# Performance work log

Measured on AMD Instinct MI355X. Metric: run time of the kernel, lower is better.

## Reference

```python
import jax, jax.numpy as jnp
import numpy as np

D_MODEL = 1024
NUM_HEADS = 16
HEAD_DIM = D_MODEL // NUM_HEADS
B, L = 2, 2048


def apply_rope(x, pos_emb):
    # x: [B,H,L,Dh], pos_emb: [1,1,L,Dh]
    x_even = x[..., ::2]
    x_odd = x[..., 1::2]
    cos = pos_emb[..., ::2]
    sin = pos_emb[..., 1::2]
    return jnp.concatenate([x_even * cos - x_odd * sin,
                            x_even * sin + x_odd * cos], axis=-1)


def setup_inputs() -> dict:
    key = jax.random.key(0)
    ks = jax.random.split(key, 13)
    s = D_MODEL ** -0.5
    return {
        'query': jax.random.normal(ks[0], (B, L, D_MODEL), jnp.float32),
        'key': jax.random.normal(ks[1], (B, L, D_MODEL), jnp.float32),
        'value': jax.random.normal(ks[2], (B, L, D_MODEL), jnp.float32),
        'alibi_bias': jax.random.normal(ks[3], (NUM_HEADS, L, L), jnp.float32),
        'pos_emb': jax.random.normal(ks[4], (1, 1, L, HEAD_DIM), jnp.float32),
        'Wq': jax.random.normal(ks[5], (D_MODEL, D_MODEL), jnp.float32) * s,
        'bq': jnp.zeros((D_MODEL,), jnp.float32),
        'Wk': jax.random.normal(ks[6], (D_MODEL, D_MODEL), jnp.float32) * s,
        'bk': jnp.zeros((D_MODEL,), jnp.float32),
        'Wv': jax.random.normal(ks[7], (D_MODEL, D_MODEL), jnp.float32) * s,
        'bv': jnp.zeros((D_MODEL,), jnp.float32),
        'Wo': jax.random.normal(ks[8], (D_MODEL, D_MODEL), jnp.float32) * s,
        'bo': jnp.zeros((D_MODEL,), jnp.float32),
    }


def reference(query, key, value, alibi_bias, pos_emb,
              Wq, bq, Wk, bk, Wv, bv, Wo, bo):
    scaling = HEAD_DIM ** -0.5
    Bq, Lq, _ = query.shape

    def proj(x, W, b):
        # torch Linear: x @ W.T + b -> [B,H,L,Dh]
        y = x @ W.T + b
        return y.reshape(Bq, Lq, NUM_HEADS, HEAD_DIM).transpose(0, 2, 1, 3)

    q = proj(query, Wq, bq)
    k = proj(key, Wk, bk)
    v = proj(value, Wv, bv)

    q = apply_rope(q, pos_emb)
    k = apply_rope(k, pos_emb)

    scores = jnp.einsum('bhqd,bhkd->bhqk', q, k) * scaling
    scores = scores + alibi_bias[None]
    attn = jax.nn.softmax(scores, axis=-1)
    out = jnp.einsum('bhqk,bhkd->bhqd', attn, v)
    out = out.transpose(0, 2, 1, 3).reshape(Bq, Lq, D_MODEL)
    return out @ Wo.T + bo
```

## Files before the change

### kernel.cpp

```cpp
#include <hip/hip_runtime.h>
#include <hip/hip_bf16.h>

#define DM 1024
#define NH 16
#define HD 64
#define BB 2
#define LLEN 2048
#define MR (BB*LLEN)

typedef __attribute__((ext_vector_type(8))) short bf16x8;
typedef __attribute__((ext_vector_type(4))) float f32x4;

#define AS1(p) ((const __attribute__((address_space(1))) void*)(p))
#define AS3(p) ((__attribute__((address_space(3))) void*)(p))

__device__ __forceinline__ ushort f2bf(float x) {
    union { float f; unsigned u; } v; v.f = x;
    unsigned r = v.u + 0x7FFFu + ((v.u >> 16) & 1u);
    return (ushort)(r >> 16);
}
__device__ __forceinline__ float bf2f(ushort x) {
    union { unsigned u; float f; } v; v.u = ((unsigned)x) << 16;
    return v.f;
}

__global__ __launch_bounds__(256) void cvtX(const float* __restrict__ a,
                                            const float* __restrict__ b,
                                            const float* __restrict__ c,
                                            ushort* __restrict__ dst, int n) {
    const float* src = blockIdx.y == 0 ? a : (blockIdx.y == 1 ? b : c);
    ushort* d = dst + (size_t)blockIdx.y * n;
    int i = (blockIdx.x * 256 + threadIdx.x) * 4;
    float4 v = *(const float4*)(src + i);
    ushort4 o = make_ushort4(f2bf(v.x), f2bf(v.y), f2bf(v.z), f2bf(v.w));
    *(ushort4*)(d + i) = o;
}

__global__ __launch_bounds__(256) void cvtW(const float* __restrict__ w0,
                                            const float* __restrict__ w1,
                                            const float* __restrict__ w2,
                                            const float* __restrict__ w3,
                                            ushort* __restrict__ dst, int n) {
    const float* src = blockIdx.y == 0 ? w0 : (blockIdx.y == 1 ? w1 : (blockIdx.y == 2 ? w2 : w3));
    ushort* d = dst + (size_t)blockIdx.y * n;
    int i = (blockIdx.x * 256 + threadIdx.x) * 4;
    float4 v = *(const float4*)(src + i);
    ushort4 o = make_ushort4(f2bf(v.x), f2bf(v.y), f2bf(v.z), f2bf(v.w));
    *(ushort4*)(d + i) = o;
}

template<typename OutT>
__global__ __launch_bounds__(256) void gemm_bt(
    const ushort* __restrict__ A, const ushort* __restrict__ Bw,
    OutT* __restrict__ Cc,
    const float* __restrict__ bias0, const float* __restrict__ bias1, const float* __restrict__ bias2,
    int M, int N, int K, long sA, long sB, long sC)
{
    __shared__ __attribute__((aligned(16))) ushort As[128 * 32];
    __shared__ __attribute__((aligned(16))) ushort Bs[128 * 32];
    const int tid = threadIdx.x;
    const int lane = tid & 63;
    const int wv = tid >> 6;
    const int wm = wv >> 1, wn = wv & 1;
    const int z = blockIdx.z;
    const ushort* Ab = A + (size_t)z * sA;
    const ushort* Bb = Bw + (size_t)z * sB;
    OutT* Cb = Cc + (size_t)z * sC;
    const float* bias = z == 0 ? bias0 : (z == 1 ? bias1 : bias2);
    const int m0 = blockIdx.x * 128;
    const int n0 = blockIdx.y * 128;
    const int l15 = lane & 15, l4 = lane >> 4;

    f32x4 acc[4][4] = {};
    const int nk = K >> 5;
    const int srow = tid >> 2;
    const int sblk = tid & 3;

    auto stage = [&](int kb) {
        int k0 = kb * 32;
#pragma unroll
        for (int r = 0; r < 2; ++r) {
            int row = r * 64 + srow;
            int s = (row >> 1) & 3;
            const ushort* ga = Ab + (size_t)(m0 + row) * K + k0 + ((sblk ^ s) * 8);
            __builtin_amdgcn_global_load_lds(AS1(ga), AS3(As + row * 32 + sblk * 8), 16, 0, 0);
            const ushort* gb = Bb + (size_t)(n0 + row) * K + k0 + ((sblk ^ s) * 8);
            __builtin_amdgcn_global_load_lds(AS1(gb), AS3(Bs + row * 32 + sblk * 8), 16, 0, 0);
        }
    };

    stage(0);
    for (int kb = 0; kb < nk; ++kb) {
        __syncthreads();
        bf16x8 af[4], bfr[4];
#pragma unroll
        for (int i = 0; i < 4; ++i) {
            int rowA = wm * 64 + i * 16 + l15;
            int sa = (rowA >> 1) & 3;
            af[i] = *(const bf16x8*)(As + rowA * 32 + ((l4 ^ sa) * 8));
            int rowB = wn * 64 + i * 16 + l15;
            int sb = (rowB >> 1) & 3;
            bfr[i] = *(const bf16x8*)(Bs + rowB * 32 + ((l4 ^ sb) * 8));
        }
#pragma unroll
        for (int i = 0; i < 4; ++i)
#pragma unroll
            for (int j = 0; j < 4; ++j)
                acc[i][j] = __builtin_amdgcn_mfma_f32_16x16x32_bf16(af[i], bfr[j], acc[i][j], 0, 0, 0);
        __syncthreads();
        if (kb + 1 < nk) stage(kb + 1);
    }
#pragma unroll
    for (int i = 0; i < 4; ++i) {
#pragma unroll
        for (int j = 0; j < 4; ++j) {
            int col = n0 + wn * 64 + j * 16 + l15;
            float bv = bias[col];
#pragma unroll
            for (int r = 0; r < 4; ++r) {
                int row = m0 + wm * 64 + i * 16 + l4 * 4 + r;
                float val = acc[i][j][r] + bv;
                if constexpr (sizeof(OutT) == 2) {
                    ((ushort*)Cb)[(size_t)row * N + col] = f2bf(val);
                } else {
                    Cb[(size_t)row * N + col] = val;
                }
            }
        }
    }
}

__global__ __launch_bounds__(256) void rope_qk(const ushort* __restrict__ Yq,
                                               const ushort* __restrict__ Yk,
                                               const float* __restrict__ pe,
                                               ushort* __restrict__ Qr,
                                               ushort* __restrict__ Kr) {
    const float QS = 0.125f * 1.44269504f;
    int idx = blockIdx.x * 256 + threadIdx.x;
    int t = idx & 31;
    int h = (idx >> 5) & 15;
    int lq = (idx >> 9) & 2047;
    int b = idx >> 20;
    size_t srcoff = ((size_t)(b * LLEN + lq)) * DM + h * 64 + 2 * t;
    float2 cs = *(const float2*)(pe + (size_t)lq * 64 + 2 * t);
    unsigned yq = *(const unsigned*)(Yq + srcoff);
    unsigned yk = *(const unsigned*)(Yk + srcoff);
    float qe = bf2f((ushort)(yq & 0xffff)), qo = bf2f((ushort)(yq >> 16));
    float ke = bf2f((ushort)(yk & 0xffff)), ko = bf2f((ushort)(yk >> 16));
    size_t dst = ((size_t)(b * NH + h) * LLEN + lq) * 64;
    Qr[dst + t]      = f2bf((qe * cs.x - qo * cs.y) * QS);
    Qr[dst + 32 + t] = f2bf((qe * cs.y + qo * cs.x) * QS);
    Kr[dst + t]      = f2bf(ke * cs.x - ko * cs.y);
    Kr[dst + 32 + t] = f2bf(ke * cs.y + ko * cs.x);
}

__global__ __launch_bounds__(256) void vtrans(const ushort* __restrict__ Yv, ushort* __restrict__ Vt) {
    __shared__ __attribute__((aligned(16))) ushort Vs[64 * 66];
    int tid = threadIdx.x;
    int lb = blockIdx.x * 64;
    int bh = blockIdx.y;
    int b = bh >> 4, h = bh & 15;
#pragma unroll
    for (int p = 0; p < 2; ++p) {
        int lr = p * 32 + (tid >> 3);
        int cb = tid & 7;
        bf16x8 v = *(const bf16x8*)(Yv + (size_t)(b * LLEN + lb + lr) * DM + h * 64 + cb * 8);
#pragma unroll
        for (int j = 0; j < 8; ++j)
            Vs[(cb * 8 + j) * 66 + lr] = (ushort)v[j];
    }
    __syncthreads();
    int d = tid >> 2, part = tid & 3;
    unsigned w[8];
#pragma unroll
    for (int i = 0; i < 8; ++i) {
        unsigned lo = Vs[d * 66 + part * 16 + 2 * i];
        unsigned hi = Vs[d * 66 + part * 16 + 2 * i + 1];
        w[i] = lo | (hi << 16);
    }
    size_t dst = ((size_t)(bh * 64 + d)) * LLEN + lb + part * 16;
    uint4 o0 = make_uint4(w[0], w[1], w[2], w[3]);
    uint4 o1 = make_uint4(w[4], w[5], w[6], w[7]);
    *(uint4*)(Vt + dst) = o0;
    *(uint4*)(Vt + dst + 8) = o1;
}

__global__ __launch_bounds__(256, 8) void attn(
    const ushort* __restrict__ Qr, const ushort* __restrict__ Kr, const ushort* __restrict__ Vt,
    const float* __restrict__ alibi, float* __restrict__ O1, float* __restrict__ O2,
    float2* __restrict__ Ml)
{
    __shared__ __attribute__((aligned(16))) ushort Ps[4][16 * 72];
    const float LOG2E = 1.44269504f;
    int tid = threadIdx.x, lane = tid & 63, w = tid >> 6;
    int l15 = lane & 15, l4 = lane >> 4;
    int b = w >> 1, wq = w & 1;
    int h = blockIdx.y;
    int z = blockIdx.z;
    int qb = blockIdx.x * 32 + wq * 16;
    int bh = b * NH + h;
    int kb0 = z * (LLEN / 2);

    const ushort* Qb = Qr + ((size_t)bh * LLEN) * 64;
    const ushort* Kb = Kr + ((size_t)bh * LLEN) * 64;
    const ushort* Vb = Vt + ((size_t)bh * 64) * LLEN;
    const float* ab = alibi + (size_t)h * LLEN * LLEN;

    bf16x8 qf0 = *(const bf16x8*)(Qb + (size_t)(qb + l15) * 64 + l4 * 8);
    bf16x8 qf1 = *(const bf16x8*)(Qb + (size_t)(qb + l15) * 64 + 32 + l4 * 8);

    f32x4 O[4] = {};
    float mreg[4] = {-1e30f, -1e30f, -1e30f, -1e30f};
    float lreg[4] = {0.f, 0.f, 0.f, 0.f};
    ushort* Pw = &Ps[w][0];

    for (int kb = kb0; kb < kb0 + LLEN / 2; kb += 64) {
        f32x4 s[4];
#pragma unroll
        for (int t = 0; t < 4; ++t) {
            const ushort* kr = Kb + (size_t)(kb + t * 16 + l15) * 64;
            bf16x8 kf0 = *(const bf16x8*)(kr + l4 * 8);
            bf16x8 kf1 = *(const bf16x8*)(kr + 32 + l4 * 8);
            f32x4 zz = {};
            zz = __builtin_amdgcn_mfma_f32_16x16x32_bf16(qf0, kf0, zz, 0, 0, 0);
            s[t] = __builtin_amdgcn_mfma_f32_16x16x32_bf16(qf1, kf1, zz, 0, 0, 0);
        }
        float sv[4][4];
#pragma unroll
        for (int t = 0; t < 4; ++t) {
            const float* ar = ab + (size_t)(qb + l4 * 4) * LLEN + kb + t * 16 + l15;
#pragma unroll
            for (int r = 0; r < 4; ++r)
                sv[t][r] = fmaf(ar[(size_t)r * LLEN], LOG2E, s[t][r]);
        }
        float fac[4];
#pragma unroll
        for (int r = 0; r < 4; ++r) {
            float mx = fmaxf(fmaxf(sv[0][r], sv[1][r]), fmaxf(sv[2][r], sv[3][r]));
            mx = fmaxf(mx, __shfl_xor(mx, 1));
            mx = fmaxf(mx, __shfl_xor(mx, 2));
            mx = fmaxf(mx, __shfl_xor(mx, 4));
            mx = fmaxf(mx, __shfl_xor(mx, 8));
            float mnew = fmaxf(mreg[r], mx);
            fac[r] = exp2f(mreg[r] - mnew);
            mreg[r] = mnew;
        }
#pragma unroll
        for (int r = 0; r < 4; ++r) {
            float rs = 0.f;
#pragma unroll
            for (int t = 0; t < 4; ++t) {
                float p = exp2f(sv[t][r] - mreg[r]);
                sv[t][r] = p;
                rs += p;
            }
            rs += __shfl_xor(rs, 1);
            rs += __shfl_xor(rs, 2);
            rs += __shfl_xor(rs, 4);
            rs += __shfl_xor(rs, 8);
            lreg[r] = lreg[r] * fac[r] + rs;
        }
#pragma unroll
        for (int t = 0; t < 4; ++t)
#pragma unroll
            for (int r = 0; r < 4; ++r)
                Pw[(l4 * 4 + r) * 72 + t * 16 + l15] = f2bf(sv[t][r]);
#pragma unroll
        for (int dt = 0; dt < 4; ++dt)
#pragma unroll
            for (int r = 0; r < 4; ++r)
                O[dt][r] *= fac[r];
        bf16x8 pf0 = *(const bf16x8*)(Pw + l15 * 72 + l4 * 8);
        bf16x8 pf1 = *(const bf16x8*)(Pw + l15 * 72 + 32 + l4 * 8);
#pragma unroll
        for (int dt = 0; dt < 4; ++dt) {
            const ushort* vr = Vb + (size_t)(dt * 16 + l15) * LLEN + kb;
            bf16x8 vf0 = *(const bf16x8*)(vr + l4 * 8);
            bf16x8 vf1 = *(const bf16x8*)(vr + 32 + l4 * 8);
            O[dt] = __builtin_amdgcn_mfma_f32_16x16x32_bf16(pf0, vf0, O[dt], 0, 0, 0);
            O[dt] = __builtin_amdgcn_mfma_f32_16x16x32_bf16(pf1, vf1, O[dt], 0, 0, 0);
        }
    }
    float* Op = (z == 0) ? O1 : O2;
#pragma unroll
    for (int dt = 0; dt < 4; ++dt)
#pragma unroll
        for (int r = 0; r < 4; ++r) {
            int q = qb + l4 * 4 + r;
            Op[((size_t)bh * LLEN + q) * 64 + dt * 16 + l15] = O[dt][r];
        }
    if (l15 == 0) {
#pragma unroll
        for (int r = 0; r < 4; ++r) {
            int q = qb + l4 * 4 + r;
            Ml[((size_t)z * BB * NH + bh) * LLEN + q] = make_float2(mreg[r], lreg[r]);
        }
    }
}

__global__ __launch_bounds__(256) void combine(
    const float* __restrict__ O1, const float* __restrict__ O2,
    const float2* __restrict__ Ml, ushort* __restrict__ Abuf)
{
    int idx = blockIdx.x * 256 + threadIdx.x;
    int d4 = idx & 15;
    int q  = (idx >> 4) & (LLEN - 1);
    int bh = idx >> 15;
    int b = bh >> 4, h = bh & 15;
    float2 ml1 = Ml[(size_t)bh * LLEN + q];
    float2 ml2 = Ml[(size_t)(BB * NH + bh) * LLEN + q];
    float m = fmaxf(ml1.x, ml2.x);
    float w1 = exp2f(ml1.x - m);
    float w2 = exp2f(ml2.x - m);
    float inv = 1.0f / (ml1.y * w1 + ml2.y * w2);
    size_t off = ((size_t)bh * LLEN + q) * 64 + d4 * 4;
    float4 a = *(const float4*)(O1 + off);
    float4 c = *(const float4*)(O2 + off);
    ushort4 o;
    o.x = f2bf((a.x * w1 + c.x * w2) * inv);
    o.y = f2bf((a.y * w1 + c.y * w2) * inv);
    o.z = f2bf((a.z * w1 + c.z * w2) * inv);
    o.w = f2bf((a.w * w1 + c.w * w2) * inv);
    *(ushort4*)(Abuf + ((size_t)(b * LLEN + q)) * DM + h * 64 + d4 * 4) = o;
}

extern "C" void kernel_launch(void* const* d_in, const int* in_sizes, int n_in,
                              void* d_out, int out_size, void* d_ws, size_t ws_size,
                              hipStream_t stream) {
    const float* query = (const float*)d_in[0];
    const float* key_  = (const float*)d_in[1];
    const float* value = (const float*)d_in[2];
    const float* alibi = (const float*)d_in[3];
    const float* pose  = (const float*)d_in[4];
    const float* Wq    = (const float*)d_in[5];
    const float* bq    = (const float*)d_in[6];
    const float* Wk    = (const float*)d_in[7];
    const float* bk    = (const float*)d_in[8];
    const float* Wv    = (const float*)d_in[9];
    const float* bv    = (const float*)d_in[10];
    const float* Wo    = (const float*)d_in[11];
    const float* bo    = (const float*)d_in[12];

    ushort* Xbf  = (ushort*)d_ws;
    ushort* Wbf  = Xbf + 3UL * MR * DM;
    ushort* Ybf  = Wbf + 4UL * DM * DM;
    ushort* Qr   = Ybf + 3UL * MR * DM;
    ushort* Kr   = Qr + (size_t)BB * NH * LLEN * HD;
    ushort* Vt   = Kr + (size_t)BB * NH * LLEN * HD;
    ushort* Abuf = Vt + (size_t)BB * NH * LLEN * HD;

    float*  O1 = (float*)Xbf;
    float2* Ml = (float2*)(Xbf + 9UL * 1024 * 1024);
    float*  O2 = (float*)Ybf;

    cvtX<<<dim3(4096, 3), 256, 0, stream>>>(query, key_, value, Xbf, MR * DM);
    cvtW<<<dim3(1024, 4), 256, 0, stream>>>(Wq, Wk, Wv, Wo, Wbf, DM * DM);

    gemm_bt<ushort><<<dim3(32, 8, 3), 256, 0, stream>>>(
        Xbf, Wbf, Ybf, bq, bk, bv, MR, DM, DM,
        (long)MR * DM, (long)DM * DM, (long)MR * DM);

    rope_qk<<<8192, 256, 0, stream>>>(Ybf, Ybf + (size_t)MR * DM, pose, Qr, Kr);
    vtrans<<<dim3(32, 32), 256, 0, stream>>>(Ybf + 2UL * MR * DM, Vt);

    attn<<<dim3(LLEN / 32, NH, 2), 256, 0, stream>>>(Qr, Kr, Vt, alibi, O1, O2, Ml);
    combine<<<4096, 256, 0, stream>>>(O1, O2, Ml, Abuf);

    gemm_bt<float><<<dim3(32, 8, 1), 256, 0, stream>>>(
        Abuf, Wbf + 3UL * DM * DM, (float*)d_out, bo, bo, bo, MR, DM, DM, 0, 0, 0);
}
```

Before: 839.7 us.

## Retile projection GEMM to 128x64 with K=64 stages; move Q scaling into attention

The GEMM tile changes from 128x128 with K-step 32 to 128x64 with K-step 64, using a new XOR swizzle. Each wave now owns 32 rows across all 64 columns, and the grid doubles along N. This gives more blocks, fewer barriers per K, and fewer accumulator registers, at the cost of less operand reuse per block. The Q pre-scale also moves from rope into the attention score computation, where it adds a multiply per score, and the attention kernel's launch_bounds occupancy hint is dropped.

```diff
diff --git a/kernel.cpp b/kernel.cpp
--- a/kernel.cpp
+++ b/kernel.cpp
@@ -56,69 +56,75 @@
     const float* __restrict__ bias0, const float* __restrict__ bias1, const float* __restrict__ bias2,
     int M, int N, int K, long sA, long sB, long sC)
 {
-    __shared__ __attribute__((aligned(16))) ushort As[128 * 32];
-    __shared__ __attribute__((aligned(16))) ushort Bs[128 * 32];
+    __shared__ __attribute__((aligned(16))) ushort As[128 * 64];
+    __shared__ __attribute__((aligned(16))) ushort Bs[64 * 64];
     const int tid = threadIdx.x;
     const int lane = tid & 63;
     const int wv = tid >> 6;
-    const int wm = wv >> 1, wn = wv & 1;
     const int z = blockIdx.z;
     const ushort* Ab = A + (size_t)z * sA;
     const ushort* Bb = Bw + (size_t)z * sB;
     OutT* Cb = Cc + (size_t)z * sC;
     const float* bias = z == 0 ? bias0 : (z == 1 ? bias1 : bias2);
     const int m0 = blockIdx.x * 128;
-    const int n0 = blockIdx.y * 128;
+    const int n0 = blockIdx.y * 64;
     const int l15 = lane & 15, l4 = lane >> 4;
 
-    f32x4 acc[4][4] = {};
-    const int nk = K >> 5;
-    const int srow = tid >> 2;
-    const int sblk = tid & 3;
+    f32x4 acc[2][4] = {};
+    const int nk = K >> 6;
+    const int srow = tid >> 3;
+    const int scb  = tid & 7;
 
     auto stage = [&](int kb) {
-        int k0 = kb * 32;
+        int k0 = kb * 64;
+#pragma unroll
+        for (int r = 0; r < 4; ++r) {
+            int row = r * 32 + srow;
+            const ushort* ga = Ab + (size_t)(m0 + row) * K + k0 + ((scb ^ (row & 7)) * 8);
+            __builtin_amdgcn_global_load_lds(AS1(ga), AS3(As + row * 64 + scb * 8), 16, 0, 0);
+        }
 #pragma unroll
         for (int r = 0; r < 2; ++r) {
-            int row = r * 64 + srow;
-            int s = (row >> 1) & 3;
-            const ushort* ga = Ab + (size_t)(m0 + row) * K + k0 + ((sblk ^ s) * 8);
-            __builtin_amdgcn_global_load_lds(AS1(ga), AS3(As + row * 32 + sblk * 8), 16, 0, 0);
-            const ushort* gb = Bb + (size_t)(n0 + row) * K + k0 + ((sblk ^ s) * 8);
-            __builtin_amdgcn_global_load_lds(AS1(gb), AS3(Bs + row * 32 + sblk * 8), 16, 0, 0);
+            int row = r * 32 + srow;
+            const ushort* gb = Bb + (size_t)(n0 + row) * K + k0 + ((scb ^ (row & 7)) * 8);
+            __builtin_amdgcn_global_load_lds(AS1(gb), AS3(Bs + row * 64 + scb * 8), 16, 0, 0);
         }
     };
 
     stage(0);
     for (int kb = 0; kb < nk; ++kb) {
         __syncthreads();
-        bf16x8 af[4], bfr[4];
-#pragma unroll
-        for (int i = 0; i < 4; ++i) {
-            int rowA = wm * 64 + i * 16 + l15;
-            int sa = (rowA >> 1) & 3;
-            af[i] = *(const bf16x8*)(As + rowA * 32 + ((l4 ^ sa) * 8));
-            int rowB = wn * 64 + i * 16 + l15;
-            int sb = (rowB >> 1) & 3;
-            bfr[i] = *(const bf16x8*)(Bs + rowB * 32 + ((l4 ^ sb) * 8));
-        }
-#pragma unroll
-        for (int i = 0; i < 4; ++i)
-#pragma unroll
-            for (int j = 0; j < 4; ++j)
-                acc[i][j] = __builtin_amdgcn_mfma_f32_16x16x32_bf16(af[i], bfr[j], acc[i][j], 0, 0, 0);
+#pragma unroll
+        for (int kk = 0; kk < 2; ++kk) {
+            bf16x8 af[2], bfr[4];
+#pragma unroll
+            for (int i = 0; i < 2; ++i) {
+                int row = wv * 32 + i * 16 + l15;
+                af[i] = *(const bf16x8*)(As + row * 64 + ((((kk << 2) | l4) ^ (row & 7)) * 8));
+            }
+#pragma unroll
+            for (int j = 0; j < 4; ++j) {
+                int row = j * 16 + l15;
+                bfr[j] = *(const bf16x8*)(Bs + row * 64 + ((((kk << 2) | l4) ^ (row & 7)) * 8));
+            }
+#pragma unroll
+            for (int i = 0; i < 2; ++i)
+#pragma unroll
+                for (int j = 0; j < 4; ++j)
+                    acc[i][j] = __builtin_amdgcn_mfma_f32_16x16x32_bf16(af[i], bfr[j], acc[i][j], 0, 0, 0);
+        }
         __syncthreads();
         if (kb + 1 < nk) stage(kb + 1);
     }
 #pragma unroll
-    for (int i = 0; i < 4; ++i) {
+    for (int i = 0; i < 2; ++i) {
 #pragma unroll
         for (int j = 0; j < 4; ++j) {
-            int col = n0 + wn * 64 + j * 16 + l15;
+            int col = n0 + j * 16 + l15;
             float bv = bias[col];
 #pragma unroll
             for (int r = 0; r < 4; ++r) {
-                int row = m0 + wm * 64 + i * 16 + l4 * 4 + r;
+                int row = m0 + wv * 32 + i * 16 + l4 * 4 + r;
                 float val = acc[i][j][r] + bv;
                 if constexpr (sizeof(OutT) == 2) {
                     ((ushort*)Cb)[(size_t)row * N + col] = f2bf(val);
@@ -135,7 +141,6 @@
                                                const float* __restrict__ pe,
                                                ushort* __restrict__ Qr,
                                                ushort* __restrict__ Kr) {
-    const float QS = 0.125f * 1.44269504f;
     int idx = blockIdx.x * 256 + threadIdx.x;
     int t = idx & 31;
     int h = (idx >> 5) & 15;
@@ -148,8 +153,8 @@
     float qe = bf2f((ushort)(yq & 0xffff)), qo = bf2f((ushort)(yq >> 16));
     float ke = bf2f((ushort)(yk & 0xffff)), ko = bf2f((ushort)(yk >> 16));
     size_t dst = ((size_t)(b * NH + h) * LLEN + lq) * 64;
-    Qr[dst + t]      = f2bf((qe * cs.x - qo * cs.y) * QS);
-    Qr[dst + 32 + t] = f2bf((qe * cs.y + qo * cs.x) * QS);
+    Qr[dst + t]      = f2bf(qe * cs.x - qo * cs.y);
+    Qr[dst + 32 + t] = f2bf(qe * cs.y + qo * cs.x);
     Kr[dst + t]      = f2bf(ke * cs.x - ko * cs.y);
     Kr[dst + 32 + t] = f2bf(ke * cs.y + ko * cs.x);
 }
@@ -185,13 +190,14 @@
     *(uint4*)(Vt + dst + 8) = o1;
 }
 
-__global__ __launch_bounds__(256, 8) void attn(
+__global__ __launch_bounds__(256) void attn(
     const ushort* __restrict__ Qr, const ushort* __restrict__ Kr, const ushort* __restrict__ Vt,
     const float* __restrict__ alibi, float* __restrict__ O1, float* __restrict__ O2,
     float2* __restrict__ Ml)
 {
     __shared__ __attribute__((aligned(16))) ushort Ps[4][16 * 72];
     const float LOG2E = 1.44269504f;
+    const float SC2 = 0.125f * 1.44269504f;
     int tid = threadIdx.x, lane = tid & 63, w = tid >> 6;
     int l15 = lane & 15, l4 = lane >> 4;
     int b = w >> 1, wq = w & 1;
@@ -231,7 +237,7 @@
             const float* ar = ab + (size_t)(qb + l4 * 4) * LLEN + kb + t * 16 + l15;
 #pragma unroll
             for (int r = 0; r < 4; ++r)
-                sv[t][r] = fmaf(ar[(size_t)r * LLEN], LOG2E, s[t][r]);
+                sv[t][r] = fmaf(ar[(size_t)r * LLEN], LOG2E, s[t][r] * SC2);
         }
         float fac[4];
 #pragma unroll
@@ -356,7 +362,7 @@
     cvtX<<<dim3(4096, 3), 256, 0, stream>>>(query, key_, value, Xbf, MR * DM);
     cvtW<<<dim3(1024, 4), 256, 0, stream>>>(Wq, Wk, Wv, Wo, Wbf, DM * DM);
 
-    gemm_bt<ushort><<<dim3(32, 8, 3), 256, 0, stream>>>(
+    gemm_bt<ushort><<<dim3(32, 16, 3), 256, 0, stream>>>(
         Xbf, Wbf, Ybf, bq, bk, bv, MR, DM, DM,
         (long)MR * DM, (long)DM * DM, (long)MR * DM);
 
@@ -366,6 +372,6 @@
     attn<<<dim3(LLEN / 32, NH, 2), 256, 0, stream>>>(Qr, Kr, Vt, alibi, O1, O2, Ml);
     combine<<<4096, 256, 0, stream>>>(O1, O2, Ml, Abuf);
 
-    gemm_bt<float><<<dim3(32, 8, 1), 256, 0, stream>>>(
+    gemm_bt<float><<<dim3(32, 16, 1), 256, 0, stream>>>(
         Abuf, Wbf + 3UL * DM * DM, (float*)d_out, bo, bo, bo, MR, DM, DM, 0, 0, 0);
 }
```

Measured after the change: 706.4 us. -15.9%, faster.
